# Kernel tuning notes

Hardware: AMD Instinct MI355X
Metric: run time of the kernel (lower is better)

## Reference

```python
import jax, jax.numpy as jnp
import numpy as np

N, E, IN_DIM, OUT_DIM, EDGE_DIM = 50000, 800000, 256, 128, 64
NEG_SLOPE = 0.2


def setup_inputs() -> dict:
    key = jax.random.key(0)
    ks = jax.random.split(key, 8)
    xavier = lambda k, shape: jax.random.normal(k, shape, jnp.float32) * np.float32(np.sqrt(2.0 / (shape[0] + shape[1])))
    return {
        "nfeat": jax.random.normal(ks[0], (N, IN_DIM), jnp.float32),
        "ex": jax.random.normal(ks[1], (E, EDGE_DIM), jnp.float32),
        "src": jax.random.randint(ks[2], (E,), 0, N),
        "dst": jax.random.randint(ks[3], (E,), 0, N),
        "W_fc": xavier(ks[4], (OUT_DIM, IN_DIM)),
        "b_fc": jnp.zeros((OUT_DIM,), jnp.float32),
        "W_att": xavier(ks[5], (1, 2 * OUT_DIM + EDGE_DIM)),
        "b_att": jnp.zeros((1,), jnp.float32),
        "W_edge": xavier(ks[6], (OUT_DIM, EDGE_DIM)),
        "b_edge": jnp.zeros((OUT_DIM,), jnp.float32),
        "W_eatt": xavier(ks[7], (EDGE_DIM, EDGE_DIM)),
        "b_eatt": jnp.zeros((EDGE_DIM,), jnp.float32),
    }


def reference(nfeat, ex, src, dst, W_fc, b_fc, W_att, b_att, W_edge, b_edge, W_eatt, b_eatt):
    n = nfeat.shape[0]
    # node transform: z = fc(nfeat)  [N, OUT]
    z = nfeat @ W_fc.T + b_fc
    # edge transform for attention score calc  [E, EDGE_DIM]
    ex_t = ex @ W_eatt.T + b_eatt
    z_src = z[src]                                   # [E, OUT] gather
    # attention logits on concat[z_src, z_dst, ex_t]  [E, 1]
    z2 = jnp.concatenate([z_src, z[dst], ex_t], axis=1)
    e = jax.nn.leaky_relu(z2 @ W_att.T + b_att, NEG_SLOPE)
    # edge feature message  [E, OUT]
    ez = ex @ W_edge.T + b_edge
    # segment softmax over incoming edges of each dst node
    m = jax.ops.segment_max(e, dst, num_segments=n)  # [N, 1]
    w = jnp.exp(e - m[dst])
    denom = jax.ops.segment_sum(w, dst, num_segments=n)
    alpha = w / denom[dst]                           # [E, 1]
    # h = sum_e alpha * z_src + sum_e alpha * ez (apply_attention_on_edge)
    h = jax.ops.segment_sum(alpha * (z_src + ez), dst, num_segments=n)  # [N, OUT]
    return h, alpha
```

## Files before the change

### kernel.cpp

```cpp
#include <hip/hip_runtime.h>
#include <math.h>
#include <float.h>

#define IN_D 256
#define OUT_D 128
#define ED_D 64
#define NEG 0.2f

typedef __attribute__((ext_vector_type(8))) short bf16x8;
typedef __attribute__((ext_vector_type(4))) float f32x4;

__device__ __forceinline__ unsigned short f2bf(float f) {
    unsigned u = __float_as_uint(f);
    unsigned r = (u + 0x7FFFu + ((u >> 16) & 1u)) >> 16;
    return (unsigned short)r;
}
__device__ __forceinline__ float bf2f(unsigned short h) {
    return __uint_as_float((unsigned)h << 16);
}

__global__ __launch_bounds__(256) void k_init(
        const float* __restrict__ W_att, const float* __restrict__ b_att,
        const float* __restrict__ W_eatt, const float* __restrict__ b_eatt,
        const float* __restrict__ W_fc, const float* __restrict__ W_edge,
        float* __restrict__ u, float* __restrict__ c0,
        unsigned short* __restrict__ Wb, float2* __restrict__ Wt2,
        int* __restrict__ cnt, int N) {
    int idx = blockIdx.x * 256 + threadIdx.x;
    if (idx < N) cnt[idx] = 0;
    if (idx < IN_D * OUT_D) {
        int i = idx & 7;
        int lane = (idx >> 3) & 63;
        int rest = idx >> 9;
        int nt = rest & 7, ks = rest >> 3;
        int col = nt * 16 + (lane & 15);
        int k = ks * 32 + (lane >> 4) * 8 + i;
        Wb[idx] = f2bf(W_fc[col * IN_D + k]);
    }
    if (idx < ED_D * (OUT_D / 2)) {
        int k = idx >> 6, l = idx & 63;
        Wt2[idx] = make_float2(W_edge[(2 * l) * ED_D + k], W_edge[(2 * l + 1) * ED_D + k]);
    }
    if (idx < ED_D) {
        float acc = 0.f;
        for (int j = 0; j < ED_D; ++j) acc += W_att[256 + j] * W_eatt[j * ED_D + idx];
        u[idx] = acc;
    }
    if (idx == ED_D) {
        float c = 0.f;
        for (int j = 0; j < ED_D; ++j) c += W_att[256 + j] * b_eatt[j];
        c0[0] = c + b_att[0];
    }
}

__global__ __launch_bounds__(256) void k_hist(const int* __restrict__ dst,
                                              int* __restrict__ cnt,
                                              int* __restrict__ rank, int E) {
    int i = blockIdx.x * 256 + threadIdx.x;
    if (i < E) rank[i] = atomicAdd(&cnt[dst[i]], 1);
}

#define LDA 272
__global__ __launch_bounds__(256) void k_node(
        const float* __restrict__ nfeat, const unsigned short* __restrict__ Wb,
        const float* __restrict__ b_fc, const float* __restrict__ W_att,
        unsigned short* __restrict__ zb, float* __restrict__ asrc,
        float* __restrict__ adst, int n) {
    __shared__ unsigned short sa[128 * LDA];
    int t = threadIdx.x;
    int row_base = blockIdx.x * 128;

    int r8 = t >> 3, c8 = t & 7;
#pragma unroll
    for (int p = 0; p < 4; ++p) {
        int r = p * 32 + r8;
        int node = row_base + r; if (node >= n) node = n - 1;
        const float4* srcp = (const float4*)(nfeat + (size_t)node * IN_D);
#pragma unroll
        for (int q = 0; q < 8; ++q) {
            int c4 = q * 8 + c8;
            float4 v = srcp[c4];
            unsigned pk0 = (unsigned)f2bf(v.x) | ((unsigned)f2bf(v.y) << 16);
            unsigned pk1 = (unsigned)f2bf(v.z) | ((unsigned)f2bf(v.w) << 16);
            *(uint2*)&sa[(size_t)r * LDA + c4 * 4] = make_uint2(pk0, pk1);
        }
    }
    __syncthreads();

    int lane = t & 63, w = t >> 6;
    int lr = lane & 15, lg = lane >> 4;

    f32x4 acc[2][8];
#pragma unroll
    for (int mi = 0; mi < 2; ++mi)
#pragma unroll
        for (int nt = 0; nt < 8; ++nt) acc[mi][nt] = (f32x4)(0.f);

    const bf16x8* wb8 = (const bf16x8*)Wb;
#pragma unroll
    for (int ks = 0; ks < 8; ++ks) {
        bf16x8 af[2], bfr[8];
#pragma unroll
        for (int mi = 0; mi < 2; ++mi) {
            int row = (2 * w + mi) * 16 + lr;
            af[mi] = *(const bf16x8*)&sa[(size_t)row * LDA + ks * 32 + lg * 8];
        }
#pragma unroll
        for (int nt = 0; nt < 8; ++nt)
            bfr[nt] = wb8[(ks * 8 + nt) * 64 + lane];
#pragma unroll
        for (int mi = 0; mi < 2; ++mi)
#pragma unroll
            for (int nt = 0; nt < 8; ++nt)
                acc[mi][nt] = __builtin_amdgcn_mfma_f32_16x16x32_bf16(
                    af[mi], bfr[nt], acc[mi][nt], 0, 0, 0);
    }

    float w1c[8], w2c[8], bfc[8];
#pragma unroll
    for (int nt = 0; nt < 8; ++nt) {
        int col = nt * 16 + lr;
        w1c[nt] = W_att[col];
        w2c[nt] = W_att[128 + col];
        bfc[nt] = b_fc[col];
    }
#pragma unroll
    for (int mi = 0; mi < 2; ++mi) {
        float p1[4] = {0.f, 0.f, 0.f, 0.f}, p2[4] = {0.f, 0.f, 0.f, 0.f};
#pragma unroll
        for (int nt = 0; nt < 8; ++nt) {
#pragma unroll
            for (int reg = 0; reg < 4; ++reg) {
                float zv = acc[mi][nt][reg] + bfc[nt];
                int m = row_base + (2 * w + mi) * 16 + lg * 4 + reg;
                if (m < n) zb[(size_t)m * OUT_D + nt * 16 + lr] = f2bf(zv);
                p1[reg] = fmaf(zv, w1c[nt], p1[reg]);
                p2[reg] = fmaf(zv, w2c[nt], p2[reg]);
            }
        }
#pragma unroll
        for (int reg = 0; reg < 4; ++reg) {
#pragma unroll
            for (int off = 1; off <= 8; off <<= 1) {
                p1[reg] += __shfl_xor(p1[reg], off);
                p2[reg] += __shfl_xor(p2[reg], off);
            }
        }
        if (lr == 0) {
#pragma unroll
            for (int reg = 0; reg < 4; ++reg) {
                int m = row_base + (2 * w + mi) * 16 + lg * 4 + reg;
                if (m < n) { asrc[m] = p1[reg]; adst[m] = p2[reg]; }
            }
        }
    }
}

__global__ __launch_bounds__(1024) void k_scan(const int* __restrict__ cnt,
                                               int* __restrict__ rowptr, int N) {
    int t = threadIdx.x;
    int per = (N + 1023) / 1024;
    int b0 = t * per, b1 = b0 + per;
    if (b0 > N) b0 = N;
    if (b1 > N) b1 = N;
    int s = 0;
    for (int i = b0; i < b1; ++i) s += cnt[i];
    int wl = t & 63, w = t >> 6;
    int v = s;
#pragma unroll
    for (int off = 1; off < 64; off <<= 1) {
        int a = __shfl_up(v, off);
        if (wl >= off) v += a;
    }
    __shared__ int wsum[16], woff[16];
    if (wl == 63) wsum[w] = v;
    __syncthreads();
    if (t == 0) { int r = 0; for (int i = 0; i < 16; ++i) { woff[i] = r; r += wsum[i]; } }
    __syncthreads();
    int run = woff[w] + v - s;
    for (int i = b0; i < b1; ++i) { rowptr[i] = run; run += cnt[i]; }
    if (t == 1023) rowptr[N] = run;
}

__global__ __launch_bounds__(256) void k_edge(
        const float* __restrict__ ex, const int* __restrict__ src, const int* __restrict__ dst,
        const float* __restrict__ asrc, const float* __restrict__ adst,
        const float* __restrict__ u, const float* __restrict__ c0,
        const int* __restrict__ rowptr, const int* __restrict__ rank,
        int2* __restrict__ csr, int E) {
    int i = blockIdx.x * 256 + threadIdx.x;
    if (i >= E) return;
    const float4* exr = (const float4*)(ex + (size_t)i * ED_D);
    const float4* u4 = (const float4*)u;
    float acc = 0.f;
#pragma unroll
    for (int q = 0; q < 16; ++q) {
        float4 a = exr[q], b = u4[q];
        acc += a.x * b.x + a.y * b.y + a.z * b.z + a.w * b.w;
    }
    int s = src[i], d = dst[i];
    float e = acc + asrc[s] + adst[d] + c0[0];
    e = (e > 0.f) ? e : NEG * e;
    int pos = rowptr[d] + rank[i];
    csr[pos] = make_int2(__float_as_int(e), i);
}

__global__ __launch_bounds__(256) void k_gather(
        const unsigned short* __restrict__ zb, const float2* __restrict__ ex2,
        const int* __restrict__ srcv, const int2* __restrict__ csr,
        const int* __restrict__ rowptr,
        float4* __restrict__ h4, float* __restrict__ alpha_out,
        float2* __restrict__ xsum2, int N) {
    int lane = threadIdx.x & 63;
    int half = lane >> 5, hl = lane & 31;
    int n = blockIdx.x * 4 + (threadIdx.x >> 6);
    if (n >= N) return;
    int beg = rowptr[n], end = rowptr[n + 1];
    int deg = end - beg;
    if (deg == 0) return;
    float4 accz = make_float4(0.f, 0.f, 0.f, 0.f);
    float2 accx = make_float2(0.f, 0.f);
    const ushort4* z4 = (const ushort4*)zb;

    if (deg <= 64) {
        int2 me = make_int2(0, 0);
        int sl = 0;
        float lg = -FLT_MAX;
        if (lane < deg) {
            me = csr[beg + lane];
            lg = __int_as_float(me.x);
            sl = srcv[me.y];
        }
        float m = lg;
#pragma unroll
        for (int off = 32; off >= 1; off >>= 1) m = fmaxf(m, __shfl_xor(m, off));
        float wvv = (lane < deg) ? expf(lg - m) : 0.f;
        float sw = wvv;
#pragma unroll
        for (int off = 32; off >= 1; off >>= 1) sw += __shfl_xor(sw, off);
        float al = wvv / sw;
        if (lane < deg) alpha_out[me.y] = al;
        int j = 0;
        for (; j + 8 <= deg; j += 8) {
            float a[4]; int s[4], e[4];
#pragma unroll
            for (int q = 0; q < 4; ++q) {
                int idx = j + 2 * q + half;
                a[q] = __shfl(al, idx);
                s[q] = __shfl(sl, idx);
                e[q] = __shfl(me.y, idx);
            }
            ushort4 zu[4]; float2 xv[4];
#pragma unroll
            for (int q = 0; q < 4; ++q) {
                zu[q] = z4[(size_t)s[q] * 32 + hl];
                xv[q] = ex2[(size_t)e[q] * 32 + hl];
            }
#pragma unroll
            for (int q = 0; q < 4; ++q) {
                accz.x = fmaf(a[q], bf2f(zu[q].x), accz.x);
                accz.y = fmaf(a[q], bf2f(zu[q].y), accz.y);
                accz.z = fmaf(a[q], bf2f(zu[q].z), accz.z);
                accz.w = fmaf(a[q], bf2f(zu[q].w), accz.w);
                accx.x = fmaf(a[q], xv[q].x, accx.x);
                accx.y = fmaf(a[q], xv[q].y, accx.y);
            }
        }
        if (j + 4 <= deg) {
            float a[2]; int s[2], e[2];
#pragma unroll
            for (int q = 0; q < 2; ++q) {
                int idx = j + 2 * q + half;
                a[q] = __shfl(al, idx);
                s[q] = __shfl(sl, idx);
                e[q] = __shfl(me.y, idx);
            }
            ushort4 zu[2]; float2 xv[2];
#pragma unroll
            for (int q = 0; q < 2; ++q) {
                zu[q] = z4[(size_t)s[q] * 32 + hl];
                xv[q] = ex2[(size_t)e[q] * 32 + hl];
            }
#pragma unroll
            for (int q = 0; q < 2; ++q) {
                accz.x = fmaf(a[q], bf2f(zu[q].x), accz.x);
                accz.y = fmaf(a[q], bf2f(zu[q].y), accz.y);
                accz.z = fmaf(a[q], bf2f(zu[q].z), accz.z);
                accz.w = fmaf(a[q], bf2f(zu[q].w), accz.w);
                accx.x = fmaf(a[q], xv[q].x, accx.x);
                accx.y = fmaf(a[q], xv[q].y, accx.y);
            }
            j += 4;
        }
        for (; j < deg; j += 2) {
            int idx = j + half;
            float a = __shfl(al, idx);
            int s = __shfl(sl, idx), e = __shfl(me.y, idx);
            ushort4 zu = z4[(size_t)s * 32 + hl];
            float2 xv = ex2[(size_t)e * 32 + hl];
            accz.x = fmaf(a, bf2f(zu.x), accz.x);
            accz.y = fmaf(a, bf2f(zu.y), accz.y);
            accz.z = fmaf(a, bf2f(zu.z), accz.z);
            accz.w = fmaf(a, bf2f(zu.w), accz.w);
            accx.x = fmaf(a, xv.x, accx.x);
            accx.y = fmaf(a, xv.y, accx.y);
        }
    } else {
        float m = -FLT_MAX;
        for (int c = beg + lane; c < end; c += 64)
            m = fmaxf(m, __int_as_float(csr[c].x));
#pragma unroll
        for (int off = 32; off >= 1; off >>= 1) m = fmaxf(m, __shfl_xor(m, off));
        float sw = 0.f;
        for (int c = beg + lane; c < end; c += 64)
            sw += expf(__int_as_float(csr[c].x) - m);
#pragma unroll
        for (int off = 32; off >= 1; off >>= 1) sw += __shfl_xor(sw, off);
        float rden = 1.f / sw;
        for (int c = beg; c < end; c += 64) {
            int mcnt = end - c;
            if (mcnt > 64) mcnt = 64;
            int2 me = make_int2(0, 0);
            int sl = 0;
            float al = 0.f;
            if (lane < mcnt) {
                me = csr[c + lane];
                al = expf(__int_as_float(me.x) - m) * rden;
                alpha_out[me.y] = al;
                sl = srcv[me.y];
            }
            for (int j = 0; j < mcnt; j += 2) {
                int idx = j + half;
                float a = __shfl(al, idx);
                int s = __shfl(sl, idx), e = __shfl(me.y, idx);
                ushort4 zu = z4[(size_t)s * 32 + hl];
                float2 xv = ex2[(size_t)e * 32 + hl];
                accz.x = fmaf(a, bf2f(zu.x), accz.x);
                accz.y = fmaf(a, bf2f(zu.y), accz.y);
                accz.z = fmaf(a, bf2f(zu.z), accz.z);
                accz.w = fmaf(a, bf2f(zu.w), accz.w);
                accx.x = fmaf(a, xv.x, accx.x);
                accx.y = fmaf(a, xv.y, accx.y);
            }
        }
    }
    accz.x += __shfl_xor(accz.x, 32);
    accz.y += __shfl_xor(accz.y, 32);
    accz.z += __shfl_xor(accz.z, 32);
    accz.w += __shfl_xor(accz.w, 32);
    accx.x += __shfl_xor(accx.x, 32);
    accx.y += __shfl_xor(accx.y, 32);
    if (half == 0) {
        h4[(size_t)n * 32 + hl] = accz;
        xsum2[(size_t)n * 32 + hl] = accx;
    }
}

__global__ __launch_bounds__(256) void k_xmm(
        const float2* __restrict__ Wt2, const float* __restrict__ b_edge,
        const float* __restrict__ xsum, const int* __restrict__ rowptr,
        float2* __restrict__ h2, int N) {
    __shared__ float2 swt[ED_D * 64];
    for (int i = threadIdx.x; i < ED_D * 64; i += 256) swt[i] = Wt2[i];
    __syncthreads();
    int lane = threadIdx.x & 63;
    int wv = threadIdx.x >> 6;
    float2 be2 = ((const float2*)b_edge)[lane];
    for (int n = blockIdx.x * 4 + wv; n < N; n += gridDim.x * 4) {
        int deg = rowptr[n + 1] - rowptr[n];
        if (deg == 0) {
            h2[(size_t)n * 64 + lane] = make_float2(0.f, 0.f);
            continue;
        }
        float xk = xsum[(size_t)n * 64 + lane];
        float2 hv = h2[(size_t)n * 64 + lane];
        hv.x += be2.x; hv.y += be2.y;
#pragma unroll 8
        for (int k = 0; k < 64; ++k) {
            float a = __shfl(xk, k);
            float2 w2 = swt[k * 64 + lane];
            hv.x = fmaf(a, w2.x, hv.x);
            hv.y = fmaf(a, w2.y, hv.y);
        }
        h2[(size_t)n * 64 + lane] = hv;
    }
}

extern "C" void kernel_launch(void* const* d_in, const int* in_sizes, int n_in,
                              void* d_out, int out_size, void* d_ws, size_t ws_size,
                              hipStream_t stream) {
    const float* nfeat = (const float*)d_in[0];
    const float* ex    = (const float*)d_in[1];
    const int*   src   = (const int*)d_in[2];
    const int*   dst   = (const int*)d_in[3];
    const float* W_fc  = (const float*)d_in[4];
    const float* b_fc  = (const float*)d_in[5];
    const float* W_att = (const float*)d_in[6];
    const float* b_att = (const float*)d_in[7];
    const float* W_edge = (const float*)d_in[8];
    const float* b_edge = (const float*)d_in[9];
    const float* W_eatt = (const float*)d_in[10];
    const float* b_eatt = (const float*)d_in[11];
    int N = in_sizes[0] / IN_D;
    int E = in_sizes[2];

    float* h_out = (float*)d_out;
    float* alpha_out = h_out + (size_t)N * OUT_D;

    char* w = (char*)d_ws;
    auto alloc = [&](size_t bytes) { char* p = w; w += (bytes + 255) & ~255ull; return p; };
    unsigned short* zb = (unsigned short*)alloc((size_t)N * OUT_D * 2);
    float* asrc   = (float*)alloc((size_t)N * 4);
    float* adst   = (float*)alloc((size_t)N * 4);
    int* cnt      = (int*)alloc((size_t)N * 4);
    int* rowptr   = (int*)alloc(((size_t)N + 1) * 4);
    int* rank     = (int*)alloc((size_t)E * 4);
    int2* csr     = (int2*)alloc((size_t)E * 8);
    float* xsum   = (float*)alloc((size_t)N * ED_D * 4);
    unsigned short* Wb = (unsigned short*)alloc((size_t)IN_D * OUT_D * 2);
    float2* Wt2   = (float2*)alloc((size_t)ED_D * 64 * 8);
    float* u      = (float*)alloc(64 * 4);
    float* c0     = (float*)alloc(4);

    int init_total = N > IN_D * OUT_D ? N : IN_D * OUT_D;
    k_init<<<(init_total + 255) / 256, 256, 0, stream>>>(
        W_att, b_att, W_eatt, b_eatt, W_fc, W_edge, u, c0, Wb, Wt2, cnt, N);
    k_hist<<<(E + 255) / 256, 256, 0, stream>>>(dst, cnt, rank, E);
    k_node<<<(N + 127) / 128, 256, 0, stream>>>(nfeat, Wb, b_fc, W_att, zb, asrc, adst, N);
    k_scan<<<1, 1024, 0, stream>>>(cnt, rowptr, N);
    k_edge<<<(E + 255) / 256, 256, 0, stream>>>(ex, src, dst, asrc, adst, u, c0,
                                                rowptr, rank, csr, E);
    k_gather<<<(N + 3) / 4, 256, 0, stream>>>(zb, (const float2*)ex, src, csr,
                                              rowptr, (float4*)h_out, alpha_out,
                                              (float2*)xsum, N);
    k_xmm<<<(N + 3) / 4, 256, 0, stream>>>((const float2*)Wt2, b_edge, xsum, rowptr,
                                           (float2*)h_out, N);
}
```

Before: 379.2 us.

## Write bf16 edge features in CSR order and store src in CSR entries

k_edge now converts each edge's 64-float feature row to bf16 and writes it at its CSR position, and stores the source index in a widened int4 CSR entry. k_gather then reads the edge features contiguously per destination node at half the width, and no longer does the indirect src lookup. This replaces random 256-byte gathers of fp32 ex with sequential 128-byte reads. In exchange k_edge gains 128 bytes of scattered writes per edge, the CSR array doubles in size, and edge features lose precision in the aggregation.

```diff
diff --git a/kernel.cpp b/kernel.cpp
--- a/kernel.cpp
+++ b/kernel.cpp
@@ -187,28 +187,34 @@
         const float* __restrict__ asrc, const float* __restrict__ adst,
         const float* __restrict__ u, const float* __restrict__ c0,
         const int* __restrict__ rowptr, const int* __restrict__ rank,
-        int2* __restrict__ csr, int E) {
+        int4* __restrict__ csr, uint4* __restrict__ exc, int E) {
     int i = blockIdx.x * 256 + threadIdx.x;
     if (i >= E) return;
     const float4* exr = (const float4*)(ex + (size_t)i * ED_D);
     const float4* u4 = (const float4*)u;
     float acc = 0.f;
+    unsigned pk[32];
 #pragma unroll
     for (int q = 0; q < 16; ++q) {
         float4 a = exr[q], b = u4[q];
         acc += a.x * b.x + a.y * b.y + a.z * b.z + a.w * b.w;
+        pk[2 * q]     = (unsigned)f2bf(a.x) | ((unsigned)f2bf(a.y) << 16);
+        pk[2 * q + 1] = (unsigned)f2bf(a.z) | ((unsigned)f2bf(a.w) << 16);
     }
     int s = src[i], d = dst[i];
     float e = acc + asrc[s] + adst[d] + c0[0];
     e = (e > 0.f) ? e : NEG * e;
     int pos = rowptr[d] + rank[i];
-    csr[pos] = make_int2(__float_as_int(e), i);
+    csr[pos] = make_int4(__float_as_int(e), i, s, 0);
+    uint4* dp = exc + (size_t)pos * 8;
+#pragma unroll
+    for (int q = 0; q < 8; ++q)
+        dp[q] = make_uint4(pk[4 * q], pk[4 * q + 1], pk[4 * q + 2], pk[4 * q + 3]);
 }
 
 __global__ __launch_bounds__(256) void k_gather(
-        const unsigned short* __restrict__ zb, const float2* __restrict__ ex2,
-        const int* __restrict__ srcv, const int2* __restrict__ csr,
-        const int* __restrict__ rowptr,
+        const unsigned short* __restrict__ zb, const ushort2* __restrict__ xc,
+        const int4* __restrict__ csr, const int* __restrict__ rowptr,
         float4* __restrict__ h4, float* __restrict__ alpha_out,
         float2* __restrict__ xsum2, int N) {
     int lane = threadIdx.x & 63;
@@ -223,14 +229,9 @@
     const ushort4* z4 = (const ushort4*)zb;
 
     if (deg <= 64) {
-        int2 me = make_int2(0, 0);
-        int sl = 0;
+        int4 me = make_int4(0, 0, 0, 0);
         float lg = -FLT_MAX;
-        if (lane < deg) {
-            me = csr[beg + lane];
-            lg = __int_as_float(me.x);
-            sl = srcv[me.y];
-        }
+        if (lane < deg) { me = csr[beg + lane]; lg = __int_as_float(me.x); }
         float m = lg;
 #pragma unroll
         for (int off = 32; off >= 1; off >>= 1) m = fmaxf(m, __shfl_xor(m, off));
@@ -242,19 +243,18 @@
         if (lane < deg) alpha_out[me.y] = al;
         int j = 0;
         for (; j + 8 <= deg; j += 8) {
-            float a[4]; int s[4], e[4];
+            float a[4]; int s[4];
 #pragma unroll
             for (int q = 0; q < 4; ++q) {
                 int idx = j + 2 * q + half;
                 a[q] = __shfl(al, idx);
-                s[q] = __shfl(sl, idx);
-                e[q] = __shfl(me.y, idx);
-            }
-            ushort4 zu[4]; float2 xv[4];
+                s[q] = __shfl(me.z, idx);
+            }
+            ushort4 zu[4]; ushort2 xv[4];
 #pragma unroll
             for (int q = 0; q < 4; ++q) {
                 zu[q] = z4[(size_t)s[q] * 32 + hl];
-                xv[q] = ex2[(size_t)e[q] * 32 + hl];
+                xv[q] = xc[(size_t)(beg + j + 2 * q + half) * 32 + hl];
             }
 #pragma unroll
             for (int q = 0; q < 4; ++q) {
@@ -262,24 +262,23 @@
                 accz.y = fmaf(a[q], bf2f(zu[q].y), accz.y);
                 accz.z = fmaf(a[q], bf2f(zu[q].z), accz.z);
                 accz.w = fmaf(a[q], bf2f(zu[q].w), accz.w);
-                accx.x = fmaf(a[q], xv[q].x, accx.x);
-                accx.y = fmaf(a[q], xv[q].y, accx.y);
+                accx.x = fmaf(a[q], bf2f(xv[q].x), accx.x);
+                accx.y = fmaf(a[q], bf2f(xv[q].y), accx.y);
             }
         }
         if (j + 4 <= deg) {
-            float a[2]; int s[2], e[2];
+            float a[2]; int s[2];
 #pragma unroll
             for (int q = 0; q < 2; ++q) {
                 int idx = j + 2 * q + half;
                 a[q] = __shfl(al, idx);
-                s[q] = __shfl(sl, idx);
-                e[q] = __shfl(me.y, idx);
-            }
-            ushort4 zu[2]; float2 xv[2];
+                s[q] = __shfl(me.z, idx);
+            }
+            ushort4 zu[2]; ushort2 xv[2];
 #pragma unroll
             for (int q = 0; q < 2; ++q) {
                 zu[q] = z4[(size_t)s[q] * 32 + hl];
-                xv[q] = ex2[(size_t)e[q] * 32 + hl];
+                xv[q] = xc[(size_t)(beg + j + 2 * q + half) * 32 + hl];
             }
 #pragma unroll
             for (int q = 0; q < 2; ++q) {
@@ -287,23 +286,23 @@
                 accz.y = fmaf(a[q], bf2f(zu[q].y), accz.y);
                 accz.z = fmaf(a[q], bf2f(zu[q].z), accz.z);
                 accz.w = fmaf(a[q], bf2f(zu[q].w), accz.w);
-                accx.x = fmaf(a[q], xv[q].x, accx.x);
-                accx.y = fmaf(a[q], xv[q].y, accx.y);
+                accx.x = fmaf(a[q], bf2f(xv[q].x), accx.x);
+                accx.y = fmaf(a[q], bf2f(xv[q].y), accx.y);
             }
             j += 4;
         }
         for (; j < deg; j += 2) {
             int idx = j + half;
             float a = __shfl(al, idx);
-            int s = __shfl(sl, idx), e = __shfl(me.y, idx);
+            int s = __shfl(me.z, idx);
             ushort4 zu = z4[(size_t)s * 32 + hl];
-            float2 xv = ex2[(size_t)e * 32 + hl];
+            ushort2 xv = xc[(size_t)(beg + idx) * 32 + hl];
             accz.x = fmaf(a, bf2f(zu.x), accz.x);
             accz.y = fmaf(a, bf2f(zu.y), accz.y);
             accz.z = fmaf(a, bf2f(zu.z), accz.z);
             accz.w = fmaf(a, bf2f(zu.w), accz.w);
-            accx.x = fmaf(a, xv.x, accx.x);
-            accx.y = fmaf(a, xv.y, accx.y);
+            accx.x = fmaf(a, bf2f(xv.x), accx.x);
+            accx.y = fmaf(a, bf2f(xv.y), accx.y);
         }
     } else {
         float m = -FLT_MAX;
@@ -320,27 +319,25 @@
         for (int c = beg; c < end; c += 64) {
             int mcnt = end - c;
             if (mcnt > 64) mcnt = 64;
-            int2 me = make_int2(0, 0);
-            int sl = 0;
+            int4 me = make_int4(0, 0, 0, 0);
             float al = 0.f;
             if (lane < mcnt) {
                 me = csr[c + lane];
                 al = expf(__int_as_float(me.x) - m) * rden;
                 alpha_out[me.y] = al;
-                sl = srcv[me.y];
             }
             for (int j = 0; j < mcnt; j += 2) {
                 int idx = j + half;
                 float a = __shfl(al, idx);
-                int s = __shfl(sl, idx), e = __shfl(me.y, idx);
+                int s = __shfl(me.z, idx);
                 ushort4 zu = z4[(size_t)s * 32 + hl];
-                float2 xv = ex2[(size_t)e * 32 + hl];
+                ushort2 xv = xc[(size_t)(c + idx) * 32 + hl];
                 accz.x = fmaf(a, bf2f(zu.x), accz.x);
                 accz.y = fmaf(a, bf2f(zu.y), accz.y);
                 accz.z = fmaf(a, bf2f(zu.z), accz.z);
                 accz.w = fmaf(a, bf2f(zu.w), accz.w);
-                accx.x = fmaf(a, xv.x, accx.x);
-                accx.y = fmaf(a, xv.y, accx.y);
+                accx.x = fmaf(a, bf2f(xv.x), accx.x);
+                accx.y = fmaf(a, bf2f(xv.y), accx.y);
             }
         }
     }
@@ -415,7 +412,8 @@
     int* cnt      = (int*)alloc((size_t)N * 4);
     int* rowptr   = (int*)alloc(((size_t)N + 1) * 4);
     int* rank     = (int*)alloc((size_t)E * 4);
-    int2* csr     = (int2*)alloc((size_t)E * 8);
+    int4* csr     = (int4*)alloc((size_t)E * 16);
+    uint4* exc    = (uint4*)alloc(((size_t)E + 2) * 128);
     float* xsum   = (float*)alloc((size_t)N * ED_D * 4);
     unsigned short* Wb = (unsigned short*)alloc((size_t)IN_D * OUT_D * 2);
     float2* Wt2   = (float2*)alloc((size_t)ED_D * 64 * 8);
@@ -429,9 +427,9 @@
     k_node<<<(N + 127) / 128, 256, 0, stream>>>(nfeat, Wb, b_fc, W_att, zb, asrc, adst, N);
     k_scan<<<1, 1024, 0, stream>>>(cnt, rowptr, N);
     k_edge<<<(E + 255) / 256, 256, 0, stream>>>(ex, src, dst, asrc, adst, u, c0,
-                                                rowptr, rank, csr, E);
-    k_gather<<<(N + 3) / 4, 256, 0, stream>>>(zb, (const float2*)ex, src, csr,
-                                              rowptr, (float4*)h_out, alpha_out,
+                                                rowptr, rank, csr, exc, E);
+    k_gather<<<(N + 3) / 4, 256, 0, stream>>>(zb, (const ushort2*)exc, csr, rowptr,
+                                              (float4*)h_out, alpha_out,
                                               (float2*)xsum, N);
     k_xmm<<<(N + 3) / 4, 256, 0, stream>>>((const float2*)Wt2, b_edge, xsum, rowptr,
                                            (float2*)h_out, N);
```

After: 405.9 us. 1.07x slower.

## Fuse edge logit computation into per-node gather kernel, replace edge kernel with CSR fill

Applied to the files above, without the earlier changes.

The separate per-edge logit kernel, which read all of ex (800k x 64 floats) and wrote a packed logit/id CSR, is removed. A lightweight fill kernel now writes only edge-id and source-id CSR arrays. The gather kernel computes each edge's ex·u dot product itself, using half-wave shuffle reductions, before the softmax. Because the ex rows are read again in the aggregation loop right afterwards, the aim is for that second read to hit cache and save a full DRAM pass over ex plus the logit writes. The trade-off is extra shuffle reductions per edge inside the gather, plus a high-degree path that uses an online softmax and recomputes the logits.

```diff
diff --git a/kernel.cpp b/kernel.cpp
--- a/kernel.cpp
+++ b/kernel.cpp
@@ -182,35 +182,26 @@
     if (t == 1023) rowptr[N] = run;
 }
 
-__global__ __launch_bounds__(256) void k_edge(
-        const float* __restrict__ ex, const int* __restrict__ src, const int* __restrict__ dst,
+__global__ __launch_bounds__(256) void k_fill(
+        const int* __restrict__ dst, const int* __restrict__ src,
+        const int* __restrict__ rank, const int* __restrict__ rowptr,
+        int* __restrict__ eid_csr, int* __restrict__ src_csr, int E) {
+    int i = blockIdx.x * 256 + threadIdx.x;
+    if (i >= E) return;
+    int d = dst[i];
+    int pos = rowptr[d] + rank[i];
+    eid_csr[pos] = i;
+    src_csr[pos] = src[i];
+}
+
+__global__ __launch_bounds__(256) void k_fused(
+        const unsigned short* __restrict__ zb, const float* __restrict__ ex,
+        const int* __restrict__ eid_csr, const int* __restrict__ src_csr,
+        const int* __restrict__ rowptr,
         const float* __restrict__ asrc, const float* __restrict__ adst,
         const float* __restrict__ u, const float* __restrict__ c0,
-        const int* __restrict__ rowptr, const int* __restrict__ rank,
-        int2* __restrict__ csr, int E) {
-    int i = blockIdx.x * 256 + threadIdx.x;
-    if (i >= E) return;
-    const float4* exr = (const float4*)(ex + (size_t)i * ED_D);
-    const float4* u4 = (const float4*)u;
-    float acc = 0.f;
-#pragma unroll
-    for (int q = 0; q < 16; ++q) {
-        float4 a = exr[q], b = u4[q];
-        acc += a.x * b.x + a.y * b.y + a.z * b.z + a.w * b.w;
-    }
-    int s = src[i], d = dst[i];
-    float e = acc + asrc[s] + adst[d] + c0[0];
-    e = (e > 0.f) ? e : NEG * e;
-    int pos = rowptr[d] + rank[i];
-    csr[pos] = make_int2(__float_as_int(e), i);
-}
-
-__global__ __launch_bounds__(256) void k_gather(
-        const unsigned short* __restrict__ zb, const float2* __restrict__ ex2,
-        const int* __restrict__ srcv, const int2* __restrict__ csr,
-        const int* __restrict__ rowptr,
-        float4* __restrict__ h4, float* __restrict__ alpha_out,
-        float2* __restrict__ xsum2, int N) {
+        float* __restrict__ h, float* __restrict__ alpha_out,
+        float* __restrict__ xsum, int N) {
     int lane = threadIdx.x & 63;
     int half = lane >> 5, hl = lane & 31;
     int n = blockIdx.x * 4 + (threadIdx.x >> 6);
@@ -218,18 +209,38 @@
     int beg = rowptr[n], end = rowptr[n + 1];
     int deg = end - beg;
     if (deg == 0) return;
-    float4 accz = make_float4(0.f, 0.f, 0.f, 0.f);
-    float2 accx = make_float2(0.f, 0.f);
+    float adn = adst[n], cc = c0[0];
+    const float2* ex2 = (const float2*)ex;
     const ushort4* z4 = (const ushort4*)zb;
 
     if (deg <= 64) {
-        int2 me = make_int2(0, 0);
-        int sl = 0;
+        int el = 0, sl = 0;
+        if (lane < deg) {
+            el = eid_csr[beg + lane];
+            sl = src_csr[beg + lane];
+        }
+        float2 u2 = ((const float2*)u)[hl];
         float lg = -FLT_MAX;
+        for (int j = 0; j < deg; j += 2) {
+            int j1 = (j + 1 < deg) ? j + 1 : j;
+            int e0 = __shfl(el, j), e1 = __shfl(el, j1);
+            int eh = half ? e1 : e0;
+            float2 xv = ex2[(size_t)eh * 32 + hl];
+            float d = fmaf(xv.x, u2.x, xv.y * u2.y);
+            d += __shfl_xor(d, 16);
+            d += __shfl_xor(d, 8);
+            d += __shfl_xor(d, 4);
+            d += __shfl_xor(d, 2);
+            d += __shfl_xor(d, 1);
+            float dox = __shfl_xor(d, 32);
+            float dj  = half ? dox : d;
+            float dj1 = half ? d : dox;
+            if (lane == j) lg = dj;
+            if (lane == j + 1 && j + 1 < deg) lg = dj1;
+        }
         if (lane < deg) {
-            me = csr[beg + lane];
-            lg = __int_as_float(me.x);
-            sl = srcv[me.y];
+            lg += asrc[sl] + adn + cc;
+            lg = (lg > 0.f) ? lg : NEG * lg;
         }
         float m = lg;
 #pragma unroll
@@ -239,7 +250,9 @@
 #pragma unroll
         for (int off = 32; off >= 1; off >>= 1) sw += __shfl_xor(sw, off);
         float al = wvv / sw;
-        if (lane < deg) alpha_out[me.y] = al;
+        if (lane < deg) alpha_out[el] = al;
+        float4 accz = make_float4(0.f, 0.f, 0.f, 0.f);
+        float2 accx = make_float2(0.f, 0.f);
         int j = 0;
         for (; j + 8 <= deg; j += 8) {
             float a[4]; int s[4], e[4];
@@ -248,7 +261,7 @@
                 int idx = j + 2 * q + half;
                 a[q] = __shfl(al, idx);
                 s[q] = __shfl(sl, idx);
-                e[q] = __shfl(me.y, idx);
+                e[q] = __shfl(el, idx);
             }
             ushort4 zu[4]; float2 xv[4];
 #pragma unroll
@@ -273,7 +286,7 @@
                 int idx = j + 2 * q + half;
                 a[q] = __shfl(al, idx);
                 s[q] = __shfl(sl, idx);
-                e[q] = __shfl(me.y, idx);
+                e[q] = __shfl(el, idx);
             }
             ushort4 zu[2]; float2 xv[2];
 #pragma unroll
@@ -295,7 +308,7 @@
         for (; j < deg; j += 2) {
             int idx = j + half;
             float a = __shfl(al, idx);
-            int s = __shfl(sl, idx), e = __shfl(me.y, idx);
+            int s = __shfl(sl, idx), e = __shfl(el, idx);
             ushort4 zu = z4[(size_t)s * 32 + hl];
             float2 xv = ex2[(size_t)e * 32 + hl];
             accz.x = fmaf(a, bf2f(zu.x), accz.x);
@@ -305,54 +318,53 @@
             accx.x = fmaf(a, xv.x, accx.x);
             accx.y = fmaf(a, xv.y, accx.y);
         }
+        accz.x += __shfl_xor(accz.x, 32);
+        accz.y += __shfl_xor(accz.y, 32);
+        accz.z += __shfl_xor(accz.z, 32);
+        accz.w += __shfl_xor(accz.w, 32);
+        accx.x += __shfl_xor(accx.x, 32);
+        accx.y += __shfl_xor(accx.y, 32);
+        if (half == 0) {
+            ((float4*)h)[(size_t)n * 32 + hl] = accz;
+            ((float2*)xsum)[(size_t)n * 32 + hl] = accx;
+        }
     } else {
-        float m = -FLT_MAX;
-        for (int c = beg + lane; c < end; c += 64)
-            m = fmaxf(m, __int_as_float(csr[c].x));
-#pragma unroll
-        for (int off = 32; off >= 1; off >>= 1) m = fmaxf(m, __shfl_xor(m, off));
-        float sw = 0.f;
-        for (int c = beg + lane; c < end; c += 64)
-            sw += expf(__int_as_float(csr[c].x) - m);
-#pragma unroll
-        for (int off = 32; off >= 1; off >>= 1) sw += __shfl_xor(sw, off);
-        float rden = 1.f / sw;
-        for (int c = beg; c < end; c += 64) {
-            int mcnt = end - c;
-            if (mcnt > 64) mcnt = 64;
-            int2 me = make_int2(0, 0);
-            int sl = 0;
-            float al = 0.f;
-            if (lane < mcnt) {
-                me = csr[c + lane];
-                al = expf(__int_as_float(me.x) - m) * rden;
-                alpha_out[me.y] = al;
-                sl = srcv[me.y];
-            }
-            for (int j = 0; j < mcnt; j += 2) {
-                int idx = j + half;
-                float a = __shfl(al, idx);
-                int s = __shfl(sl, idx), e = __shfl(me.y, idx);
-                ushort4 zu = z4[(size_t)s * 32 + hl];
-                float2 xv = ex2[(size_t)e * 32 + hl];
-                accz.x = fmaf(a, bf2f(zu.x), accz.x);
-                accz.y = fmaf(a, bf2f(zu.y), accz.y);
-                accz.z = fmaf(a, bf2f(zu.z), accz.z);
-                accz.w = fmaf(a, bf2f(zu.w), accz.w);
-                accx.x = fmaf(a, xv.x, accx.x);
-                accx.y = fmaf(a, xv.y, accx.y);
-            }
-        }
-    }
-    accz.x += __shfl_xor(accz.x, 32);
-    accz.y += __shfl_xor(accz.y, 32);
-    accz.z += __shfl_xor(accz.z, 32);
-    accz.w += __shfl_xor(accz.w, 32);
-    accx.x += __shfl_xor(accx.x, 32);
-    accx.y += __shfl_xor(accx.y, 32);
-    if (half == 0) {
-        h4[(size_t)n * 32 + hl] = accz;
-        xsum2[(size_t)n * 32 + hl] = accx;
+        float uv = u[lane];
+        float m = -FLT_MAX, ssum = 0.f;
+        for (int i = beg; i < end; ++i) {
+            int e = eid_csr[i];
+            float xv = ex[(size_t)e * ED_D + lane];
+            float p = xv * uv;
+#pragma unroll
+            for (int off = 32; off >= 1; off >>= 1) p += __shfl_xor(p, off);
+            float lg = p + asrc[src_csr[i]] + adn + cc;
+            lg = (lg > 0.f) ? lg : NEG * lg;
+            float mn = fmaxf(m, lg);
+            ssum = ssum * expf(m - mn) + expf(lg - mn);
+            m = mn;
+        }
+        float rden = 1.f / ssum;
+        const ushort2* z2 = (const ushort2*)zb;
+        float2 accz2 = make_float2(0.f, 0.f);
+        float accxs = 0.f;
+        for (int i = beg; i < end; ++i) {
+            int e = eid_csr[i];
+            int s = src_csr[i];
+            float xv = ex[(size_t)e * ED_D + lane];
+            float p = xv * uv;
+#pragma unroll
+            for (int off = 32; off >= 1; off >>= 1) p += __shfl_xor(p, off);
+            float lg = p + asrc[s] + adn + cc;
+            lg = (lg > 0.f) ? lg : NEG * lg;
+            float al = expf(lg - m) * rden;
+            if (lane == 0) alpha_out[e] = al;
+            accxs = fmaf(al, xv, accxs);
+            ushort2 zz = z2[(size_t)s * ED_D + lane];
+            accz2.x = fmaf(al, bf2f(zz.x), accz2.x);
+            accz2.y = fmaf(al, bf2f(zz.y), accz2.y);
+        }
+        ((float2*)h)[(size_t)n * ED_D + lane] = accz2;
+        xsum[(size_t)n * ED_D + lane] = accxs;
     }
 }
 
@@ -415,7 +427,8 @@
     int* cnt      = (int*)alloc((size_t)N * 4);
     int* rowptr   = (int*)alloc(((size_t)N + 1) * 4);
     int* rank     = (int*)alloc((size_t)E * 4);
-    int2* csr     = (int2*)alloc((size_t)E * 8);
+    int* eid_csr  = (int*)alloc((size_t)E * 4);
+    int* src_csr  = (int*)alloc((size_t)E * 4);
     float* xsum   = (float*)alloc((size_t)N * ED_D * 4);
     unsigned short* Wb = (unsigned short*)alloc((size_t)IN_D * OUT_D * 2);
     float2* Wt2   = (float2*)alloc((size_t)ED_D * 64 * 8);
@@ -428,11 +441,9 @@
     k_hist<<<(E + 255) / 256, 256, 0, stream>>>(dst, cnt, rank, E);
     k_node<<<(N + 127) / 128, 256, 0, stream>>>(nfeat, Wb, b_fc, W_att, zb, asrc, adst, N);
     k_scan<<<1, 1024, 0, stream>>>(cnt, rowptr, N);
-    k_edge<<<(E + 255) / 256, 256, 0, stream>>>(ex, src, dst, asrc, adst, u, c0,
-                                                rowptr, rank, csr, E);
-    k_gather<<<(N + 3) / 4, 256, 0, stream>>>(zb, (const float2*)ex, src, csr,
-                                              rowptr, (float4*)h_out, alpha_out,
-                                              (float2*)xsum, N);
+    k_fill<<<(E + 255) / 256, 256, 0, stream>>>(dst, src, rank, rowptr, eid_csr, src_csr, E);
+    k_fused<<<(N + 3) / 4, 256, 0, stream>>>(zb, ex, eid_csr, src_csr, rowptr, asrc, adst,
+                                             u, c0, h_out, alpha_out, xsum, N);
     k_xmm<<<(N + 3) / 4, 256, 0, stream>>>((const float2*)Wt2, b_edge, xsum, rowptr,
                                            (float2*)h_out, N);
 }
```

Result: faster. 359.4 us (-5.2%).
